# Kernel optimization log

Measured on AMD Instinct MI355X. Metric: run time of the kernel, lower is better.

## Reference

```python
import jax, jax.numpy as jnp
import numpy as np

# Config constants (match init_kwargs)
CONV_RADIUS = 0.2            # conv_radius * rigid_scale
KERNEL_RADIUS = 0.1          # kernel_radius * query_scale
RECEP_RADIUS = 0.1           # kernel_point_receptive_radius * query_scale
K_NEIGH = 32                 # neighbor_limits
INF = 1000000.0


def _gather_neighbors(points_bcn, idx, pad_val):
    # points_bcn: (B, C, N); idx: (B, N, K) with value N meaning 'shadow' pad row
    p = jnp.transpose(points_bcn, (0, 2, 1))  # (B, N, C)
    pad = jnp.full((p.shape[0], 1, p.shape[2]), pad_val, p.dtype)
    p = jnp.concatenate([p, pad], axis=1)  # (B, N+1, C)
    return jax.vmap(lambda pp, ii: pp[ii])(p, idx)  # (B, N, K, C)


def setup_inputs() -> dict:
    key = jax.random.key(0)
    ks = jax.random.split(key, 12)
    B, N, C, R, TD = 4, 4096, 128, 4, 128
    pos = jax.random.uniform(ks[0], (B, 3, N), dtype=jnp.float32)
    feat = jax.random.normal(ks[1], (B, C, N), dtype=jnp.float32)
    # kernel points: center + R points on a sphere of KERNEL_RADIUS (load_kernels 'center' fixing)
    dirs = np.array([[1, 1, 1], [1, -1, -1], [-1, 1, -1], [-1, -1, 1]], np.float32) / np.sqrt(3.0)
    kp = np.concatenate([np.zeros((1, 3), np.float32), KERNEL_RADIUS * dirs], axis=0)  # (R+1, 3)
    query_pos = jnp.asarray(kp.T)[None, :, None, :]  # (1, 3, 1, R+1)
    s = 1.0 / np.sqrt(C)
    w_begin = jax.random.normal(ks[2], (C, C), jnp.float32) * s
    b_begin = jax.random.normal(ks[3], (C,), jnp.float32) * s
    kp_weight = jax.random.normal(ks[4], (R + 1, C, C), jnp.float32) * s
    kp_bias = jax.random.normal(ks[5], (C,), jnp.float32) * s
    w_end = jax.random.normal(ks[6], (C, C), jnp.float32) * s
    b_end = jax.random.normal(ks[7], (C,), jnp.float32) * s
    cin = 3 * C + 3
    w_mlp1 = jax.random.normal(ks[8], (2 * C, cin), jnp.float32) / np.sqrt(cin)
    b_mlp1 = jax.random.normal(ks[9], (2 * C,), jnp.float32) * s
    w_mlp2 = jax.random.normal(ks[10], (TD, 2 * C), jnp.float32) / np.sqrt(2 * C)
    b_mlp2 = jax.random.normal(ks[11], (TD,), jnp.float32) * s
    return dict(pos=pos, feat=feat, query_pos=query_pos, w_begin=w_begin, b_begin=b_begin,
                kp_weight=kp_weight, kp_bias=kp_bias, w_end=w_end, b_end=b_end,
                w_mlp1=w_mlp1, b_mlp1=b_mlp1, w_mlp2=w_mlp2, b_mlp2=b_mlp2)


def reference(pos, feat, query_pos, w_begin, b_begin, kp_weight, kp_bias, w_end, b_end,
              w_mlp1, b_mlp1, w_mlp2, b_mlp2):
    B, _, N = pos.shape
    R1 = query_pos.shape[-1]  # r + 1
    R = R1 - 1
    posT = jnp.transpose(pos, (0, 2, 1))  # (B, N, 3)
    # ball query: full pairwise sq-dist + mask + sort (as in the torch module)
    norms = jnp.sum(posT * posT, axis=-1)  # (B, N)
    sqd = norms[:, :, None] + norms[:, None, :] - 2.0 * jnp.einsum('bnc,bmc->bnm', posT, posT)
    base = jnp.arange(N, dtype=jnp.int32)[None, None, :]
    idx = jnp.where(sqd > CONV_RADIUS ** 2, N, base)
    idx = jnp.sort(idx, axis=-1)[:, :, :K_NEIGH]  # (B, N, K)
    # relative neighbor positions (shadow -> INF)
    npos = _gather_neighbors(pos, idx, INF)  # (B, N, K, 3)
    rel = jnp.transpose(npos, (0, 3, 1, 2)) - pos[:, :, :, None]  # (B, 3, N, K)
    # kernel-point correlation weights
    diff = rel[..., None] - query_pos[:, :, :, None, :]  # (B, 3, N, K, R+1)
    sqd_kp = jnp.sum(diff * diff, axis=1)  # (B, N, K, R+1)
    w = jnp.clip(1.0 - jnp.sqrt(sqd_kp) / RECEP_RADIUS, 0.0, None)
    w = jnp.transpose(w, (0, 1, 3, 2))  # (B, N, R+1, K)
    # begin 1x1 conv then gather (shadow -> 0)
    feat0 = jnp.einsum('oc,bcn->bon', w_begin, feat) + b_begin[None, :, None]
    nfeat = _gather_neighbors(feat0, idx, 0.0)  # (B, N, K, C)
    wf = jnp.einsum('bnrk,bnkc->bnrc', w, nfeat)  # (B, N, R+1, C)
    qf = jnp.einsum('bnkc,kcd->bnd', wf, kp_weight) + kp_bias  # (B, N, C)
    qf = jnp.transpose(qf, (0, 2, 1))  # (B, C, N)
    qf = jax.nn.relu(qf)
    qf = jax.nn.relu(jnp.einsum('oc,bcn->bon', w_end, qf) + b_end[None, :, None] + feat)
    # build query MLP input, dropping the center kernel point (index 0)
    wf_t = jnp.transpose(wf, (0, 3, 1, 2))[:, :, :, 1:]  # (B, C, N, R)
    qp_rep = jnp.broadcast_to(query_pos, (B, 3, N, R1))[:, :, :, 1:]  # (B, 3, N, R)
    qf_rep = jnp.broadcast_to(qf[..., None], (B, qf.shape[1], N, R))
    feat_rep = jnp.broadcast_to(feat[..., None], (B, feat.shape[1], N, R))
    cat = jnp.concatenate([wf_t, qp_rep, qf_rep, feat_rep], axis=1)  # (B, 3C+3, N, R)
    h = jax.nn.relu(jnp.einsum('oc,bcnr->bonr', w_mlp1, cat) + b_mlp1[None, :, None, None])
    queries = jax.nn.relu(jnp.einsum('oc,bcnr->bonr', w_mlp2, h) + b_mlp2[None, :, None, None])
    return (query_pos[0, :, 0, 1:], queries)
```

## Files before the change

### kernel.cpp

```cpp
#include <hip/hip_runtime.h>

typedef unsigned short ushort_t;
typedef __attribute__((ext_vector_type(8))) short s8v;
typedef __attribute__((ext_vector_type(4))) float f4v;

#define NPT  4096
#define NC   128
#define NK   32
#define CIN  387
#define KPAD 416
#define WFR  136
#define WFP  680

__device__ __forceinline__ float bf2f(ushort_t u) {
    unsigned int x = ((unsigned int)u) << 16; float f; __builtin_memcpy(&f, &x, 4); return f;
}
__device__ __forceinline__ ushort_t f2bf(float f) {
    unsigned int x; __builtin_memcpy(&x, &f, 4);
    unsigned int r = x + 0x7fffu + ((x >> 16) & 1u);
    return (ushort_t)(r >> 16);
}
__device__ __forceinline__ void splitbf(float x, ushort_t& h, ushort_t& l) {
    h = f2bf(x);
    l = f2bf(x - bf2f(h));
}

__global__ __launch_bounds__(256) void k_prep(const float* qp, const float* kpw,
                                              const float* w1, const float* wend,
                                              const float* w2, const float* wb, float* out0,
                                              ushort_t* kpwT_hi, ushort_t* kpwT_lo,
                                              ushort_t* w1_hi, ushort_t* w1_lo,
                                              ushort_t* we_hi, ushort_t* we_lo,
                                              ushort_t* w2_hi, ushort_t* w2_lo,
                                              float* wbT) {
    int i = blockIdx.x * blockDim.x + threadIdx.x;
    int stride = gridDim.x * blockDim.x;
    if (i < 12) { int c = i >> 2, r = (i & 3) + 1; out0[i] = qp[c * 5 + r]; }
    for (int e = i; e < 128 * WFP; e += stride) {
        int d = e / WFP, rem = e - d * WFP;
        int r = rem / WFR, c = rem - r * WFR;
        float v = (c < 128) ? kpw[(r * 128 + c) * 128 + d] : 0.0f;
        splitbf(v, kpwT_hi[e], kpwT_lo[e]);
    }
    for (int e = i; e < 256 * KPAD; e += stride) {
        int j = e / KPAD, cn = e - j * KPAD;
        float v = 0.0f;
        if (cn < 131)       v = w1[j * CIN + cn];
        else if (cn >= 160) v = w1[j * CIN + cn - 29];
        splitbf(v, w1_hi[e], w1_lo[e]);
    }
    for (int e = i; e < 128 * 128; e += stride) splitbf(wend[e], we_hi[e], we_lo[e]);
    for (int e = i; e < 128 * 256; e += stride) splitbf(w2[e],   w2_hi[e], w2_lo[e]);
    for (int e = i; e < 128 * 128; e += stride) {
        int k = e >> 7, c = e & 127;
        wbT[e] = wb[c * 128 + k];
    }
}

__global__ __launch_bounds__(256) void k_neigh(const float* pos, int* idxg) {
    __shared__ float px[NPT], py[NPT], pz[NPT];
    int b = blockIdx.x >> 8;
    int tile = blockIdx.x & 255;
    const float* pb = pos + (size_t)b * 3 * NPT;
    for (int i = threadIdx.x; i < NPT; i += 256) {
        px[i] = pb[i];
        py[i] = pb[NPT + i];
        pz[i] = pb[2 * NPT + i];
    }
    __syncthreads();
    const double R2 = 0.2 * 0.2;
    int wave = threadIdx.x >> 6, lane = threadIdx.x & 63;
    unsigned long long below = (1ull << lane) - 1ull;
    for (int wp = 0; wp < 4; ++wp) {
        int n = tile * 16 + wave * 4 + wp;
        size_t bn = (size_t)b * NPT + n;
        double pnx = (double)px[n], pny = (double)py[n], pnz = (double)pz[n];
        double nn = pnx * pnx + pny * pny + pnz * pnz;
        int count = 0;
        for (int m0 = 0; m0 < NPT && count < NK; m0 += 64) {
            int m = m0 + lane;
            double qx = (double)px[m], qy = (double)py[m], qz = (double)pz[m];
            double nm = qx * qx + qy * qy + qz * qz;
            double dot = pnx * qx + pny * qy + pnz * qz;
            double sqd = (nn + nm) - 2.0 * dot;
            bool valid = !(sqd > R2);
            unsigned long long mask = __ballot(valid);
            int slot = count + __popcll(mask & below);
            if (valid && slot < NK) idxg[bn * NK + slot] = m;
            count += __popcll(mask);
        }
        int filled = count < NK ? count : NK;
        if (lane < NK && lane >= filled) idxg[bn * NK + lane] = -1;
    }
}

__global__ __launch_bounds__(128) void k_feat0(const float* feat, const float* wbT,
                                               const float* bb, float* feat0,
                                               ushort_t* featT_hi, ushort_t* featT_lo) {
    __shared__ float fl[128 * 8];
    int blk = blockIdx.x; int b = blk >> 9; int n0 = (blk & 511) * 8;
    int c = threadIdx.x;
    for (int e = c; e < 1024; e += 128) {
        int k = e >> 3, i = e & 7;
        fl[k * 8 + i] = feat[((size_t)b * NC + k) * NPT + n0 + i];
    }
    __syncthreads();
    for (int e = c; e < 1024; e += 128) {
        int i = e >> 7, k = e & 127;
        ushort_t h, l;
        splitbf(fl[k * 8 + i], h, l);
        size_t o = ((size_t)b * NPT + n0 + i) * NC + k;
        featT_hi[o] = h; featT_lo[o] = l;
    }
    float acc[8];
    float bv = bb[c];
    for (int i = 0; i < 8; ++i) acc[i] = bv;
    for (int k = 0; k < NC; ++k) {
        float w = wbT[k * 128 + c];
        for (int i = 0; i < 8; ++i) acc[i] = fmaf(w, fl[k * 8 + i], acc[i]);
    }
    for (int i = 0; i < 8; ++i)
        feat0[((size_t)b * NPT + n0 + i) * NC + c] = acc[i];
}

__global__ __launch_bounds__(256, 3) void k_fused(
    const float* pos, const float* qp,
    const float* feat, const float* feat0, const int* idxg,
    const ushort_t* featT_hi, const ushort_t* featT_lo,
    const ushort_t* kpwT_hi, const ushort_t* kpwT_lo, const float* kp_bias,
    const ushort_t* we_hi, const ushort_t* we_lo, const float* b_end,
    const ushort_t* w1_hi, const ushort_t* w1_lo, const float* b1,
    const ushort_t* w2_hi, const ushort_t* w2_lo, const float* b2,
    float* outq)
{
    __shared__ __align__(16) char smem[53760];
    float*    wls   = (float*)smem;
    ushort_t* q_hi  = (ushort_t*)smem;
    ushort_t* q_lo  = (ushort_t*)(smem + 4352);
    ushort_t* wf_hi = (ushort_t*)(smem + 10240);
    ushort_t* wf_lo = (ushort_t*)(smem + 32000);
    ushort_t* h_hi  = (ushort_t*)(smem + 10240);
    ushort_t* h_lo  = (ushort_t*)(smem + 27648);

    const int tid = threadIdx.x;
    const int lane = tid & 63, wv = tid >> 6;
    const int l15 = lane & 15, quad = lane >> 4;
    const int p0 = blockIdx.x * 16;
    const int bL = p0 >> 12;
    const int nb = p0 & (NPT - 1);
    const int plq = l15 >> 2;
    const int rr  = (l15 & 3) + 1;

    for (int e = tid; e < 512; e += 256) {
        int p = e >> 5, k = e & 31;
        int m = idxg[(size_t)p0 * NK + e];
        float w5[5];
        if (m < 0) {
            for (int r = 0; r < 5; ++r) w5[r] = 0.0f;
        } else {
            int n = nb + p;
            const float* pb = pos + (size_t)bL * 3 * NPT;
            float pnx = pb[n], pny = pb[NPT + n], pnz = pb[2 * NPT + n];
            float qx = pb[m], qy = pb[NPT + m], qz = pb[2 * NPT + m];
            float rx = __fsub_rn(qx, pnx), ry = __fsub_rn(qy, pny), rz = __fsub_rn(qz, pnz);
            for (int r = 0; r < 5; ++r) {
                float kx = qp[r], ky = qp[5 + r], kz = qp[10 + r];
                float dx = __fsub_rn(rx, kx), dy = __fsub_rn(ry, ky), dz = __fsub_rn(rz, kz);
                float s = __fadd_rn(__fadd_rn(__fmul_rn(dx, dx), __fmul_rn(dy, dy)), __fmul_rn(dz, dz));
                float w = 1.0f - __fdiv_rn(__fsqrt_rn(s), 0.1f);
                w5[r] = fmaxf(w, 0.0f);
            }
        }
        for (int r = 0; r < 5; ++r) wls[p * 160 + r * 32 + k] = w5[r];
    }
    __syncthreads();

    int idxA = idxg[(size_t)(p0 + wv * 4) * NK + lane];
    int idxB = idxg[(size_t)(p0 + wv * 4) * NK + 64 + lane];
    for (int pp = 0; pp < 4; ++pp) {
        int p = wv * 4 + pp;
        int src = (pp < 2) ? idxA : idxB;
        int blane = (pp & 1) * 32;
        float a0[5], a1[5];
        for (int r = 0; r < 5; ++r) { a0[r] = 0.f; a1[r] = 0.f; }
        for (int k = 0; k < NK; ++k) {
            int m = __shfl(src, blane + k);
            int mc = m < 0 ? 0 : m;
            const float* fp = feat0 + (((size_t)bL << 12) + mc) * NC + (lane << 1);
            float v0 = fp[0], v1 = fp[1];
            for (int r = 0; r < 5; ++r) {
                float w = wls[p * 160 + r * 32 + k];
                a0[r] = fmaf(w, v0, a0[r]);
                a1[r] = fmaf(w, v1, a1[r]);
            }
        }
        for (int r = 0; r < 5; ++r) {
            ushort_t h0, l0, h1, l1;
            splitbf(a0[r], h0, l0); splitbf(a1[r], h1, l1);
            int off = p * WFP + r * WFR + (lane << 1);
            *(unsigned int*)(wf_hi + off) = (unsigned int)h0 | ((unsigned int)h1 << 16);
            *(unsigned int*)(wf_lo + off) = (unsigned int)l0 | ((unsigned int)l1 << 16);
        }
    }
    __syncthreads();

    f4v ch[2], cm[2], cl[2];
    for (int nt = 0; nt < 2; ++nt) { ch[nt] = (f4v){0,0,0,0}; cm[nt] = (f4v){0,0,0,0}; cl[nt] = (f4v){0,0,0,0}; }
    for (int r = 0; r < 5; ++r)
        for (int kt = 0; kt < 4; ++kt) {
            int ao = l15 * WFP + r * WFR + kt * 32 + quad * 8;
            s8v ah = *(const s8v*)(wf_hi + ao);
            s8v al = *(const s8v*)(wf_lo + ao);
            for (int nt = 0; nt < 2; ++nt) {
                size_t ro = (size_t)(wv * 32 + nt * 16 + l15) * WFP + r * WFR + kt * 32 + quad * 8;
                s8v bh = *(const s8v*)(kpwT_hi + ro);
                s8v bl = *(const s8v*)(kpwT_lo + ro);
                ch[nt] = __builtin_amdgcn_mfma_f32_16x16x32_bf16(ah, bh, ch[nt], 0, 0, 0);
                cm[nt] = __builtin_amdgcn_mfma_f32_16x16x32_bf16(ah, bl, cm[nt], 0, 0, 0);
                cl[nt] = __builtin_amdgcn_mfma_f32_16x16x32_bf16(al, bh, cl[nt], 0, 0, 0);
            }
        }
    __syncthreads();
    for (int nt = 0; nt < 2; ++nt) {
        int d = wv * 32 + nt * 16 + l15;
        float bias = kp_bias[d];
        f4v c1 = (ch[nt] + cm[nt]) + cl[nt];
        for (int reg = 0; reg < 4; ++reg) {
            int m = quad * 4 + reg;
            ushort_t vh, vl;
            splitbf(fmaxf(c1[reg] + bias, 0.0f), vh, vl);
            q_hi[m * 136 + d] = vh; q_lo[m * 136 + d] = vl;
        }
    }
    __syncthreads();

    f4v dh[2], dm[2], dl[2];
    for (int nt = 0; nt < 2; ++nt) { dh[nt] = (f4v){0,0,0,0}; dm[nt] = (f4v){0,0,0,0}; dl[nt] = (f4v){0,0,0,0}; }
    for (int kt = 0; kt < 4; ++kt) {
        s8v ah = *(const s8v*)(q_hi + l15 * 136 + kt * 32 + quad * 8);
        s8v al = *(const s8v*)(q_lo + l15 * 136 + kt * 32 + quad * 8);
        for (int nt = 0; nt < 2; ++nt) {
            size_t ro = (size_t)(wv * 32 + nt * 16 + l15) * NC + kt * 32 + quad * 8;
            s8v bh = *(const s8v*)(we_hi + ro);
            s8v bl = *(const s8v*)(we_lo + ro);
            dh[nt] = __builtin_amdgcn_mfma_f32_16x16x32_bf16(ah, bh, dh[nt], 0, 0, 0);
            dm[nt] = __builtin_amdgcn_mfma_f32_16x16x32_bf16(ah, bl, dm[nt], 0, 0, 0);
            dl[nt] = __builtin_amdgcn_mfma_f32_16x16x32_bf16(al, bh, dl[nt], 0, 0, 0);
        }
    }
    __syncthreads();
    for (int nt = 0; nt < 2; ++nt) {
        int c = wv * 32 + nt * 16 + l15;
        float bias = b_end[c];
        f4v fv = *(const f4v*)(feat + ((size_t)(bL * NC + c)) * NPT + nb + quad * 4);
        f4v c2 = (dh[nt] + dm[nt]) + dl[nt];
        for (int reg = 0; reg < 4; ++reg) {
            int m = quad * 4 + reg;
            float v = c2[reg] + bias + fv[reg];
            ushort_t vh, vl;
            splitbf(fmaxf(v, 0.0f), vh, vl);
            q_hi[m * 136 + c] = vh; q_lo[m * 136 + c] = vl;
        }
    }
    __syncthreads();

    union { s8v v; ushort_t u[8]; } aqp_h, aqp_l;
    for (int j = 0; j < 8; ++j) { aqp_h.u[j] = 0; aqp_l.u[j] = 0; }
    if (quad == 0)
        for (int j = 0; j < 3; ++j) splitbf(qp[j * 5 + rr], aqp_h.u[j], aqp_l.u[j]);

    f4v e1[4][4];
    for (int mt = 0; mt < 4; ++mt) for (int nt = 0; nt < 4; ++nt) e1[mt][nt] = (f4v){0,0,0,0};
    #pragma unroll
    for (int kt = 0; kt < 13; ++kt) {
        s8v ah[4], al[4];
        for (int mt = 0; mt < 4; ++mt) {
            int pl = mt * 4 + plq;
            if (kt < 4) {
                int ao = pl * WFP + rr * WFR + kt * 32 + quad * 8;
                ah[mt] = *(const s8v*)(wf_hi + ao);
                al[mt] = *(const s8v*)(wf_lo + ao);
            } else if (kt == 4) {
                ah[mt] = aqp_h.v; al[mt] = aqp_l.v;
            } else if (kt < 9) {
                int ao = pl * 136 + (kt - 5) * 32 + quad * 8;
                ah[mt] = *(const s8v*)(q_hi + ao);
                al[mt] = *(const s8v*)(q_lo + ao);
            } else {
                size_t go = (size_t)(p0 + pl) * NC + (kt - 9) * 32 + quad * 8;
                ah[mt] = *(const s8v*)(featT_hi + go);
                al[mt] = *(const s8v*)(featT_lo + go);
            }
        }
        for (int nt = 0; nt < 4; ++nt) {
            size_t ro = (size_t)(wv * 64 + nt * 16 + l15) * KPAD + kt * 32 + quad * 8;
            s8v bh = *(const s8v*)(w1_hi + ro);
            s8v bl = *(const s8v*)(w1_lo + ro);
            for (int mt = 0; mt < 4; ++mt) {
                e1[mt][nt] = __builtin_amdgcn_mfma_f32_16x16x32_bf16(ah[mt], bh, e1[mt][nt], 0, 0, 0);
                e1[mt][nt] = __builtin_amdgcn_mfma_f32_16x16x32_bf16(ah[mt], bl, e1[mt][nt], 0, 0, 0);
                e1[mt][nt] = __builtin_amdgcn_mfma_f32_16x16x32_bf16(al[mt], bh, e1[mt][nt], 0, 0, 0);
            }
        }
    }
    __syncthreads();

    f4v f1[4][2];
    for (int mt = 0; mt < 4; ++mt) for (int nt = 0; nt < 2; ++nt) f1[mt][nt] = (f4v){0,0,0,0};
    for (int half = 0; half < 2; ++half) {
        if ((wv >> 1) == half) {
            for (int nt = 0; nt < 4; ++nt) {
                int j = wv * 64 + nt * 16 + l15;
                int col = j - half * 128;
                float bias = b1[j];
                for (int mt = 0; mt < 4; ++mt)
                    for (int reg = 0; reg < 4; ++reg) {
                        int m = mt * 16 + quad * 4 + reg;
                        ushort_t vh, vl;
                        splitbf(fmaxf(e1[mt][nt][reg] + bias, 0.0f), vh, vl);
                        h_hi[m * 136 + col] = vh; h_lo[m * 136 + col] = vl;
                    }
            }
        }
        __syncthreads();
        for (int kt = half * 4; kt < half * 4 + 4; ++kt) {
            int lcol = kt * 32 + quad * 8 - half * 128;
            s8v ah[4], al[4];
            for (int mt = 0; mt < 4; ++mt) {
                ah[mt] = *(const s8v*)(h_hi + (mt * 16 + l15) * 136 + lcol);
                al[mt] = *(const s8v*)(h_lo + (mt * 16 + l15) * 136 + lcol);
            }
            for (int nt = 0; nt < 2; ++nt) {
                size_t ro = (size_t)(wv * 32 + nt * 16 + l15) * 256 + kt * 32 + quad * 8;
                s8v bh = *(const s8v*)(w2_hi + ro);
                s8v bl = *(const s8v*)(w2_lo + ro);
                for (int mt = 0; mt < 4; ++mt) {
                    f1[mt][nt] = __builtin_amdgcn_mfma_f32_16x16x32_bf16(ah[mt], bh, f1[mt][nt], 0, 0, 0);
                    f1[mt][nt] = __builtin_amdgcn_mfma_f32_16x16x32_bf16(ah[mt], bl, f1[mt][nt], 0, 0, 0);
                    f1[mt][nt] = __builtin_amdgcn_mfma_f32_16x16x32_bf16(al[mt], bh, f1[mt][nt], 0, 0, 0);
                }
            }
        }
        __syncthreads();
    }
    for (int nt = 0; nt < 2; ++nt) {
        int d = wv * 32 + nt * 16 + l15;
        float bias = b2[d];
        for (int mt = 0; mt < 4; ++mt) {
            int m0 = mt * 16 + quad * 4;
            int pt = m0 >> 2;
            int n = nb + pt;
            f4v vv;
            for (int reg = 0; reg < 4; ++reg)
                vv[reg] = fmaxf(f1[mt][nt][reg] + bias, 0.0f);
            *(f4v*)(outq + ((size_t)(bL * 128 + d) * NPT + n) * 4) = vv;
        }
    }
}

extern "C" void kernel_launch(void* const* d_in, const int* in_sizes, int n_in,
                              void* d_out, int out_size, void* d_ws, size_t ws_size,
                              hipStream_t stream) {
    const float* pos     = (const float*)d_in[0];
    const float* feat    = (const float*)d_in[1];
    const float* qp      = (const float*)d_in[2];
    const float* w_begin = (const float*)d_in[3];
    const float* b_begin = (const float*)d_in[4];
    const float* kp_w    = (const float*)d_in[5];
    const float* kp_b    = (const float*)d_in[6];
    const float* w_end   = (const float*)d_in[7];
    const float* b_end   = (const float*)d_in[8];
    const float* w_mlp1  = (const float*)d_in[9];
    const float* b_mlp1  = (const float*)d_in[10];
    const float* w_mlp2  = (const float*)d_in[11];
    const float* b_mlp2  = (const float*)d_in[12];
    float* out = (float*)d_out;

    char* ws = (char*)d_ws;
    int*      idxg     = (int*)     (ws + 0);
    float*    feat0    = (float*)   (ws + 2097152);
    ushort_t* featT_hi = (ushort_t*)(ws + 10485760);
    ushort_t* featT_lo = (ushort_t*)(ws + 14680064);
    ushort_t* kpwT_hi  = (ushort_t*)(ws + 18874368);
    ushort_t* kpwT_lo  = (ushort_t*)(ws + 19048448);
    ushort_t* w1_hi    = (ushort_t*)(ws + 19222528);
    ushort_t* w1_lo    = (ushort_t*)(ws + 19435520);
    ushort_t* we_hi    = (ushort_t*)(ws + 19648512);
    ushort_t* we_lo    = (ushort_t*)(ws + 19681280);
    ushort_t* w2_hi    = (ushort_t*)(ws + 19714048);
    ushort_t* w2_lo    = (ushort_t*)(ws + 19779584);
    float*    wbT      = (float*)   (ws + 19845120);

    k_prep <<<512,  256, 0, stream>>>(qp, kp_w, w_mlp1, w_end, w_mlp2, w_begin, out,
                                      kpwT_hi, kpwT_lo, w1_hi, w1_lo, we_hi, we_lo,
                                      w2_hi, w2_lo, wbT);
    k_neigh<<<1024, 256, 0, stream>>>(pos, idxg);
    k_feat0<<<2048, 128, 0, stream>>>(feat, wbT, b_begin, feat0, featT_hi, featT_lo);
    k_fused<<<1024, 256, 0, stream>>>(pos, qp, feat, feat0, idxg, featT_hi, featT_lo,
                                      kpwT_hi, kpwT_lo, kp_b, we_hi, we_lo, b_end,
                                      w1_hi, w1_lo, b_mlp1, w2_hi, w2_lo, b_mlp2, out + 12);
}
```

Before: 279.1 us.

## Merge prep, neighbor search and feat0 kernels into one multi-role launch

Combines the weight-prep, neighbor-search and begin-projection kernels into one kernel whose blocks take a role from their block index, so the three independent jobs run concurrently instead of back to back. A small transpose kernel for w_begin now runs first because the feat0 blocks read wbT. The prep branch still rewrites wbT while feat0 blocks read it; the values are identical, so the race is benign but redundant. Feat0 blocks now handle 16 points with 256 threads, and every block reserves 48KB of shared memory, which may lower occupancy for the lighter roles.

```diff
diff --git a/kernel.cpp b/kernel.cpp
--- a/kernel.cpp
+++ b/kernel.cpp
@@ -25,102 +25,111 @@
     l = f2bf(x - bf2f(h));
 }
 
-__global__ __launch_bounds__(256) void k_prep(const float* qp, const float* kpw,
-                                              const float* w1, const float* wend,
-                                              const float* w2, const float* wb, float* out0,
-                                              ushort_t* kpwT_hi, ushort_t* kpwT_lo,
-                                              ushort_t* w1_hi, ushort_t* w1_lo,
-                                              ushort_t* we_hi, ushort_t* we_lo,
-                                              ushort_t* w2_hi, ushort_t* w2_lo,
-                                              float* wbT) {
-    int i = blockIdx.x * blockDim.x + threadIdx.x;
-    int stride = gridDim.x * blockDim.x;
-    if (i < 12) { int c = i >> 2, r = (i & 3) + 1; out0[i] = qp[c * 5 + r]; }
-    for (int e = i; e < 128 * WFP; e += stride) {
-        int d = e / WFP, rem = e - d * WFP;
-        int r = rem / WFR, c = rem - r * WFR;
-        float v = (c < 128) ? kpw[(r * 128 + c) * 128 + d] : 0.0f;
-        splitbf(v, kpwT_hi[e], kpwT_lo[e]);
-    }
-    for (int e = i; e < 256 * KPAD; e += stride) {
-        int j = e / KPAD, cn = e - j * KPAD;
-        float v = 0.0f;
-        if (cn < 131)       v = w1[j * CIN + cn];
-        else if (cn >= 160) v = w1[j * CIN + cn - 29];
-        splitbf(v, w1_hi[e], w1_lo[e]);
-    }
-    for (int e = i; e < 128 * 128; e += stride) splitbf(wend[e], we_hi[e], we_lo[e]);
-    for (int e = i; e < 128 * 256; e += stride) splitbf(w2[e],   w2_hi[e], w2_lo[e]);
-    for (int e = i; e < 128 * 128; e += stride) {
-        int k = e >> 7, c = e & 127;
-        wbT[e] = wb[c * 128 + k];
-    }
-}
-
-__global__ __launch_bounds__(256) void k_neigh(const float* pos, int* idxg) {
-    __shared__ float px[NPT], py[NPT], pz[NPT];
-    int b = blockIdx.x >> 8;
-    int tile = blockIdx.x & 255;
-    const float* pb = pos + (size_t)b * 3 * NPT;
-    for (int i = threadIdx.x; i < NPT; i += 256) {
-        px[i] = pb[i];
-        py[i] = pb[NPT + i];
-        pz[i] = pb[2 * NPT + i];
-    }
-    __syncthreads();
-    const double R2 = 0.2 * 0.2;
-    int wave = threadIdx.x >> 6, lane = threadIdx.x & 63;
-    unsigned long long below = (1ull << lane) - 1ull;
-    for (int wp = 0; wp < 4; ++wp) {
-        int n = tile * 16 + wave * 4 + wp;
-        size_t bn = (size_t)b * NPT + n;
-        double pnx = (double)px[n], pny = (double)py[n], pnz = (double)pz[n];
-        double nn = pnx * pnx + pny * pny + pnz * pnz;
-        int count = 0;
-        for (int m0 = 0; m0 < NPT && count < NK; m0 += 64) {
-            int m = m0 + lane;
-            double qx = (double)px[m], qy = (double)py[m], qz = (double)pz[m];
-            double nm = qx * qx + qy * qy + qz * qz;
-            double dot = pnx * qx + pny * qy + pnz * qz;
-            double sqd = (nn + nm) - 2.0 * dot;
-            bool valid = !(sqd > R2);
-            unsigned long long mask = __ballot(valid);
-            int slot = count + __popcll(mask & below);
-            if (valid && slot < NK) idxg[bn * NK + slot] = m;
-            count += __popcll(mask);
-        }
-        int filled = count < NK ? count : NK;
-        if (lane < NK && lane >= filled) idxg[bn * NK + lane] = -1;
-    }
-}
-
-__global__ __launch_bounds__(128) void k_feat0(const float* feat, const float* wbT,
-                                               const float* bb, float* feat0,
-                                               ushort_t* featT_hi, ushort_t* featT_lo) {
-    __shared__ float fl[128 * 8];
-    int blk = blockIdx.x; int b = blk >> 9; int n0 = (blk & 511) * 8;
-    int c = threadIdx.x;
-    for (int e = c; e < 1024; e += 128) {
-        int k = e >> 3, i = e & 7;
-        fl[k * 8 + i] = feat[((size_t)b * NC + k) * NPT + n0 + i];
-    }
-    __syncthreads();
-    for (int e = c; e < 1024; e += 128) {
-        int i = e >> 7, k = e & 127;
-        ushort_t h, l;
-        splitbf(fl[k * 8 + i], h, l);
-        size_t o = ((size_t)b * NPT + n0 + i) * NC + k;
-        featT_hi[o] = h; featT_lo[o] = l;
-    }
-    float acc[8];
-    float bv = bb[c];
-    for (int i = 0; i < 8; ++i) acc[i] = bv;
-    for (int k = 0; k < NC; ++k) {
-        float w = wbT[k * 128 + c];
-        for (int i = 0; i < 8; ++i) acc[i] = fmaf(w, fl[k * 8 + i], acc[i]);
-    }
-    for (int i = 0; i < 8; ++i)
-        feat0[((size_t)b * NPT + n0 + i) * NC + c] = acc[i];
+__global__ __launch_bounds__(256) void k_front(
+    const float* pos, int* idxg,
+    const float* feat, const float* wb, const float* bb,
+    float* feat0, ushort_t* featT_hi, ushort_t* featT_lo,
+    const float* qp, const float* kpw, const float* w1, const float* wend, const float* w2,
+    float* out0,
+    ushort_t* kpwT_hi, ushort_t* kpwT_lo, ushort_t* w1_hi, ushort_t* w1_lo,
+    ushort_t* we_hi, ushort_t* we_lo, ushort_t* w2_hi, ushort_t* w2_lo, float* wbT)
+{
+    __shared__ float shp[3 * NPT];
+    int tid = threadIdx.x;
+    if (blockIdx.x < 1024) {
+        float* px = shp; float* py = shp + NPT; float* pz = shp + 2 * NPT;
+        int b = blockIdx.x >> 8;
+        int tile = blockIdx.x & 255;
+        const float* pb = pos + (size_t)b * 3 * NPT;
+        for (int i = tid; i < NPT; i += 256) {
+            px[i] = pb[i];
+            py[i] = pb[NPT + i];
+            pz[i] = pb[2 * NPT + i];
+        }
+        __syncthreads();
+        const double R2 = 0.2 * 0.2;
+        int wave = tid >> 6, lane = tid & 63;
+        unsigned long long below = (1ull << lane) - 1ull;
+        for (int wp = 0; wp < 4; ++wp) {
+            int n = tile * 16 + wave * 4 + wp;
+            size_t bn = (size_t)b * NPT + n;
+            double pnx = (double)px[n], pny = (double)py[n], pnz = (double)pz[n];
+            double nn = pnx * pnx + pny * pny + pnz * pnz;
+            int count = 0;
+            for (int m0 = 0; m0 < NPT && count < NK; m0 += 64) {
+                int m = m0 + lane;
+                double qx = (double)px[m], qy = (double)py[m], qz = (double)pz[m];
+                double nm = qx * qx + qy * qy + qz * qz;
+                double dot = pnx * qx + pny * qy + pnz * qz;
+                double sqd = (nn + nm) - 2.0 * dot;
+                bool valid = !(sqd > R2);
+                unsigned long long mask = __ballot(valid);
+                int slot = count + __popcll(mask & below);
+                if (valid && slot < NK) idxg[bn * NK + slot] = m;
+                count += __popcll(mask);
+            }
+            int filled = count < NK ? count : NK;
+            if (lane < NK && lane >= filled) idxg[bn * NK + lane] = -1;
+        }
+    } else if (blockIdx.x < 2048) {
+        float* fl = shp;
+        int fb = blockIdx.x - 1024;
+        int b = fb >> 8; int n0 = (fb & 255) * 16;
+        for (int e = tid; e < 2048; e += 256) {
+            int k = e >> 4, i = e & 15;
+            fl[k * 16 + i] = feat[((size_t)b * NC + k) * NPT + n0 + i];
+        }
+        __syncthreads();
+        for (int e = tid; e < 2048; e += 256) {
+            int i = e >> 7, k = e & 127;
+            ushort_t h, l;
+            splitbf(fl[k * 16 + i], h, l);
+            size_t o = ((size_t)b * NPT + n0 + i) * NC + k;
+            featT_hi[o] = h; featT_lo[o] = l;
+        }
+        int ch = tid & 127;
+        int ih = (tid >> 7) * 8;
+        float acc[8];
+        float bv = bb[ch];
+        for (int j = 0; j < 8; ++j) acc[j] = bv;
+        for (int k = 0; k < NC; ++k) {
+            float w = wbT[k * 128 + ch];
+            for (int j = 0; j < 8; ++j) acc[j] = fmaf(w, fl[k * 16 + ih + j], acc[j]);
+        }
+        for (int j = 0; j < 8; ++j)
+            feat0[((size_t)b * NPT + n0 + ih + j) * NC + ch] = acc[j];
+    } else {
+        int i = (blockIdx.x - 2048) * 256 + tid;
+        int stride = 512 * 256;
+        if (i < 12) { int c = i >> 2, r = (i & 3) + 1; out0[i] = qp[c * 5 + r]; }
+        for (int e = i; e < 128 * WFP; e += stride) {
+            int d = e / WFP, rem = e - d * WFP;
+            int r = rem / WFR, c = rem - r * WFR;
+            float v = (c < 128) ? kpw[(r * 128 + c) * 128 + d] : 0.0f;
+            splitbf(v, kpwT_hi[e], kpwT_lo[e]);
+        }
+        for (int e = i; e < 256 * KPAD; e += stride) {
+            int j = e / KPAD, cn = e - j * KPAD;
+            float v = 0.0f;
+            if (cn < 131)       v = w1[j * CIN + cn];
+            else if (cn >= 160) v = w1[j * CIN + cn - 29];
+            splitbf(v, w1_hi[e], w1_lo[e]);
+        }
+        for (int e = i; e < 128 * 128; e += stride) splitbf(wend[e], we_hi[e], we_lo[e]);
+        for (int e = i; e < 128 * 256; e += stride) splitbf(w2[e],   w2_hi[e], w2_lo[e]);
+        for (int e = i; e < 128 * 128; e += stride) {
+            int k = e >> 7, c = e & 127;
+            wbT[e] = wb[c * 128 + k];
+        }
+    }
+}
+
+__global__ __launch_bounds__(256) void k_wbt(const float* wb, float* wbT) {
+    int i = blockIdx.x * 256 + threadIdx.x;
+    if (i < 128 * 128) {
+        int k = i >> 7, c = i & 127;
+        wbT[i] = wb[c * 128 + k];
+    }
 }
 
 __global__ __launch_bounds__(256, 3) void k_fused(
@@ -391,11 +400,12 @@
     ushort_t* w2_lo    = (ushort_t*)(ws + 19779584);
     float*    wbT      = (float*)   (ws + 19845120);
 
-    k_prep <<<512,  256, 0, stream>>>(qp, kp_w, w_mlp1, w_end, w_mlp2, w_begin, out,
+    k_wbt  <<<64,   256, 0, stream>>>(w_begin, wbT);
+    k_front<<<2560, 256, 0, stream>>>(pos, idxg, feat, w_begin, b_begin,
+                                      feat0, featT_hi, featT_lo,
+                                      qp, kp_w, w_mlp1, w_end, w_mlp2, out,
                                       kpwT_hi, kpwT_lo, w1_hi, w1_lo, we_hi, we_lo,
                                       w2_hi, w2_lo, wbT);
-    k_neigh<<<1024, 256, 0, stream>>>(pos, idxg);
-    k_feat0<<<2048, 128, 0, stream>>>(feat, wbT, b_begin, feat0, featT_hi, featT_lo);
     k_fused<<<1024, 256, 0, stream>>>(pos, qp, feat, feat0, idxg, featT_hi, featT_lo,
                                       kpwT_hi, kpwT_lo, kp_b, we_hi, we_lo, b_end,
                                       w1_hi, w1_lo, b_mlp1, w2_hi, w2_lo, b_mlp2, out + 12);
```

Result: faster. 262.5 us (-5.9%).
